# Performance work log

Hardware: AMD Instinct MI355X
Metric: run time of the kernel (lower is better)

## Reference

```python
import jax, jax.numpy as jnp
import numpy as np

N_NODES = 50000
N_EDGES = 800000
D = 128        # in_channels == out_channels
EDGE_DIM = 32
EPS = 0.0      # GINEConv default eps


def setup_inputs() -> dict:
    key = jax.random.key(0)
    ks = jax.random.split(key, 12)
    s = lambda d: 1.0 / np.sqrt(d)
    inp = {
        "x": jax.random.normal(ks[0], (N_NODES, D), jnp.float32),
        "edge_index": jax.random.randint(ks[1], (2, N_EDGES), 0, N_NODES, jnp.int64),
        "edge_attr": jax.random.normal(ks[2], (N_EDGES, EDGE_DIM), jnp.float32),
        "importance": jax.random.uniform(ks[3], (N_NODES, 1), jnp.float32),
        # GINEConv edge lin: Linear(edge_dim, in_channels)
        "We": jax.random.uniform(ks[4], (EDGE_DIM, D), jnp.float32, -s(EDGE_DIM), s(EDGE_DIM)),
        "be": jax.random.uniform(ks[5], (D,), jnp.float32, -s(EDGE_DIM), s(EDGE_DIM)),
        # GINEConv nn: Linear(in_channels, out_channels)
        "Wc": jax.random.uniform(ks[6], (D, D), jnp.float32, -s(D), s(D)),
        "bc": jax.random.uniform(ks[7], (D,), jnp.float32, -s(D), s(D)),
        # importance_gate: Linear(out_channels + 1, out_channels)
        "Wg": jax.random.uniform(ks[8], (D + 1, D), jnp.float32, -s(D + 1), s(D + 1)),
        "bg": jax.random.uniform(ks[9], (D,), jnp.float32, -s(D + 1), s(D + 1)),
        # importance_propagation: Linear(out_channels, 1)
        "Wp": jax.random.uniform(ks[10], (D, 1), jnp.float32, -s(D), s(D)),
        "bp": jax.random.uniform(ks[11], (1,), jnp.float32, -s(D), s(D)),
    }
    return inp


def reference(x, edge_index, edge_attr, importance, We, be, Wc, bc, Wg, bg, Wp, bp):
    src, dst = edge_index[0], edge_index[1]
    # GINEConv: messages = relu(x_j + lin(edge_attr)), aggregated by sum at dst
    e = edge_attr @ We + be                      # [E, D]
    msg = jax.nn.relu(x[src] + e)                # [E, D] gather + fused add/relu
    agg = jax.ops.segment_sum(msg, dst, num_segments=N_NODES)  # [N, D] scatter-add
    conv_out = ((1.0 + EPS) * x + agg) @ Wc + bc  # [N, D]
    # importance gating + residual
    gate_in = jnp.concatenate([conv_out, importance], axis=-1)  # [N, D+1]
    gate = jax.nn.sigmoid(gate_in @ Wg + bg)
    out = gate * conv_out + (1.0 - gate) * x
    propagated_importance = out @ Wp + bp        # [N, 1]
    return (out, propagated_importance)
```

## Files before the change

kernel.cpp:

```cpp
#include <hip/hip_runtime.h>

#define NN 50000
#define NE 800000
#define DD 128
#define ED 32
#define NB 196
#define NC32 (NE / 32)

typedef short  bf16x8 __attribute__((ext_vector_type(8)));
typedef float  f32x4  __attribute__((ext_vector_type(4)));
typedef float  f32x16 __attribute__((ext_vector_type(16)));

__device__ __forceinline__ float4 ld4(const float* p) {
    return *reinterpret_cast<const float4*>(p);
}
__device__ __forceinline__ short f2bf(float f) {
    unsigned u = __float_as_uint(f);
    u += 0x7fffu + ((u >> 16) & 1u);
    return (short)(u >> 16);
}
__device__ __forceinline__ float bf2f(short h) {
    return __uint_as_float(((unsigned)(unsigned short)h) << 16);
}
__device__ __forceinline__ int sniff64(const int* ei) {
    return ((ei[1] | ei[3] | ei[5] | ei[7]) == 0) ? 1 : 0;
}

__global__ __launch_bounds__(256)
void k_xcast(const float* __restrict__ x, unsigned int* __restrict__ xb) {
    const int t = blockIdx.x * 256 + threadIdx.x;
    if (t >= NN * 32) return;
    const int n = t >> 5, c = t & 31;
    const float* xr = x + (size_t)n * DD + c;
    const unsigned b0 = (unsigned short)f2bf(xr[0]);
    const unsigned b1 = (unsigned short)f2bf(xr[32]);
    const unsigned b2 = (unsigned short)f2bf(xr[64]);
    const unsigned b3 = (unsigned short)f2bf(xr[96]);
    xb[(size_t)n * 64 + c * 2]     = b0 | (b1 << 16);
    xb[(size_t)n * 64 + c * 2 + 1] = b2 | (b3 << 16);
}

__global__ __launch_bounds__(256)
void k_hist(const int* __restrict__ ei, int* __restrict__ counts) {
    const int is64 = sniff64(ei);
    const int2* ei2 = (const int2*)ei;
    for (int e = blockIdx.x * blockDim.x + threadIdx.x; e < NE;
         e += gridDim.x * blockDim.x) {
        const int dst = is64 ? ei2[NE + e].x : ei[NE + e];
        atomicAdd(&counts[dst], 1);
    }
}

__global__ __launch_bounds__(256)
void k_bsum(const int* __restrict__ counts, int* __restrict__ bsum) {
    const int i = blockIdx.x * 256 + threadIdx.x;
    int c = (i < NN) ? counts[i] : 0;
#pragma unroll
    for (int off = 32; off; off >>= 1) c += __shfl_xor(c, off, 64);
    __shared__ int ws4[4];
    if ((threadIdx.x & 63) == 0) ws4[threadIdx.x >> 6] = c;
    __syncthreads();
    if (threadIdx.x == 0) bsum[blockIdx.x] = ws4[0] + ws4[1] + ws4[2] + ws4[3];
}

__global__ __launch_bounds__(256)
void k_scanb(const int* __restrict__ bsum, int* __restrict__ bexcl) {
    const int tid = threadIdx.x, lane = tid & 63, w = tid >> 6;
    const int v = (tid < NB) ? bsum[tid] : 0;
    int s = v;
#pragma unroll
    for (int off = 1; off < 64; off <<= 1) {
        const int t = __shfl_up(s, off, 64);
        if (lane >= off) s += t;
    }
    __shared__ int wsum[4], wexcl[4];
    if (lane == 63) wsum[w] = s;
    __syncthreads();
    if (tid == 0) {
        int r = 0;
#pragma unroll
        for (int k = 0; k < 4; ++k) { wexcl[k] = r; r += wsum[k]; }
    }
    __syncthreads();
    if (tid < NB) bexcl[tid] = wexcl[w] + s - v;
}

__global__ __launch_bounds__(256)
void k_rowptr(const int* __restrict__ counts, const int* __restrict__ bexcl,
              int* __restrict__ cursor) {
    const int tid = threadIdx.x, lane = tid & 63, w = tid >> 6;
    const int i = blockIdx.x * 256 + tid;
    const int c = (i < NN) ? counts[i] : 0;
    int s = c;
#pragma unroll
    for (int off = 1; off < 64; off <<= 1) {
        const int t = __shfl_up(s, off, 64);
        if (lane >= off) s += t;
    }
    __shared__ int wsum[4], wexcl[4];
    if (lane == 63) wsum[w] = s;
    __syncthreads();
    if (tid == 0) {
        int r = 0;
#pragma unroll
        for (int k = 0; k < 4; ++k) { wexcl[k] = r; r += wsum[k]; }
    }
    __syncthreads();
    if (i < NN) cursor[i] = bexcl[blockIdx.x] + wexcl[w] + s - c;
}

__global__ __launch_bounds__(256)
void k_scatter2(const int* __restrict__ ei, int* __restrict__ cursor,
                const float* __restrict__ ea, int* __restrict__ sdat4,
                unsigned int* __restrict__ ebs)
{
    const int tid = threadIdx.x;
    const int e0  = blockIdx.x * 128;
    __shared__ int spos[128];
    if (tid < 128) {
        const int is64 = sniff64(ei);
        const int2* ei2 = (const int2*)ei;
        const int e   = e0 + tid;
        const int src = is64 ? ei2[e].x : ei[e];
        const int dst = is64 ? ei2[NE + e].x : ei[NE + e];
        const int pos = atomicAdd(&cursor[dst], 1);
        sdat4[pos] = src | (dst << 16);
        spos[tid] = pos;
    }
    __syncthreads();
#pragma unroll
    for (int it = 0; it < 8; ++it) {
        const int task = it * 256 + tid;
        const int el   = task >> 4;
        const int part = task & 15;
        const float2 v = *reinterpret_cast<const float2*>(
                             ea + (size_t)(e0 + el) * ED + part * 2);
        const unsigned lo = (unsigned short)f2bf(v.x);
        const unsigned hi = (unsigned short)f2bf(v.y);
        ebs[(size_t)spos[el] * 16 + part] = lo | (hi << 16);
    }
}

__global__ __launch_bounds__(256, 4)
void k_aggE(const unsigned int* __restrict__ xb, const unsigned int* __restrict__ ebs,
            const float* __restrict__ We, const float* __restrict__ be,
            const int* __restrict__ sdat4, float* __restrict__ agg)
{
    const int lane = threadIdx.x & 63;
    const int col  = lane & 31;
    const int h    = lane >> 5;
    const int wid  = (blockIdx.x << 2) | (threadIdx.x >> 6);

    bf16x8 Bf[4][2];
    float  beb[4];
#pragma unroll
    for (int bb = 0; bb < 4; ++bb) {
#pragma unroll
        for (int s = 0; s < 2; ++s)
#pragma unroll
            for (int i = 0; i < 8; ++i)
                Bf[bb][s][i] = f2bf(We[(s * 16 + h * 8 + i) * DD + bb * 32 + col]);
        beb[bb] = be[bb * 32 + col];
    }

    const int sd   = sdat4[wid * 32 + col];
    const int dstv = ((unsigned)sd) >> 16;

    const unsigned int* ebr = ebs + ((size_t)wid * 32 + col) * 16;
    const bf16x8 Af0 = *reinterpret_cast<const bf16x8*>(ebr + h * 4);
    const bf16x8 Af1 = *reinterpret_cast<const bf16x8*>(ebr + 8 + h * 4);

    f32x16 C[4];
#pragma unroll
    for (int reg = 0; reg < 16; ++reg) {
        const int E   = (reg & 3) + 8 * (reg >> 2) + 4 * h;
        const int src = __shfl(sd, E, 64) & 0xFFFF;
        const uint2 w = *reinterpret_cast<const uint2*>(
                            xb + (size_t)src * 64 + col * 2);
        C[0][reg] = __uint_as_float(w.x << 16);
        C[1][reg] = __uint_as_float(w.x & 0xFFFF0000u);
        C[2][reg] = __uint_as_float(w.y << 16);
        C[3][reg] = __uint_as_float(w.y & 0xFFFF0000u);
    }

#pragma unroll
    for (int bb = 0; bb < 4; ++bb) {
        C[bb] = __builtin_amdgcn_mfma_f32_32x32x16_bf16(Af0, Bf[bb][0], C[bb], 0, 0, 0);
        C[bb] = __builtin_amdgcn_mfma_f32_32x32x16_bf16(Af1, Bf[bb][1], C[bb], 0, 0, 0);
    }

#pragma unroll
    for (int bb = 0; bb < 4; ++bb)
#pragma unroll
        for (int reg = 0; reg < 16; ++reg)
            C[bb][reg] = fmaxf(C[bb][reg] + beb[bb], 0.0f);

    const int  prv  = __shfl(dstv, (lane == 0) ? 0 : lane - 1, 64);
    const bool flag = (lane < 32) && ((col == 0) || (dstv != prv));
    unsigned rem = (unsigned)(__ballot(flag) & 0xFFFFFFFFull);

    while (rem) {
        const int ms = __ffs((int)rem) - 1;
        rem &= rem - 1;
        const int hi = rem ? (__ffs((int)rem) - 1) : 32;
        const int d  = __shfl(dstv, ms, 64);

        float v0 = 0.f, v1 = 0.f, v2 = 0.f, v3 = 0.f;
#pragma unroll
        for (int reg = 0; reg < 16; ++reg) {
            const int E = (reg & 3) + 8 * (reg >> 2) + 4 * h;
            const float mk = (E >= ms && E < hi) ? 1.0f : 0.0f;
            v0 = fmaf(mk, C[0][reg], v0);
            v1 = fmaf(mk, C[1][reg], v1);
            v2 = fmaf(mk, C[2][reg], v2);
            v3 = fmaf(mk, C[3][reg], v3);
        }
        v0 += __shfl_xor(v0, 32, 64);
        v1 += __shfl_xor(v1, 32, 64);
        v2 += __shfl_xor(v2, 32, 64);
        v3 += __shfl_xor(v3, 32, 64);

        float* ar = agg + (size_t)d * DD + h * 64 + col;
        unsafeAtomicAdd(ar,      h ? v2 : v0);
        unsafeAtomicAdd(ar + 32, h ? v3 : v1);
    }
}

__global__ __launch_bounds__(256)
void k_cg(const float* __restrict__ x, const float* agg,
          const float* __restrict__ Wc, const float* __restrict__ bc,
          const float* __restrict__ imp, const float* __restrict__ Wg,
          const float* __restrict__ bg, const float* __restrict__ Wp,
          const float* __restrict__ bp, float* outp, float* __restrict__ prop)
{
    __shared__ short sBh[2048 * 8];
    __shared__ short sBl[2048 * 8];
    for (int idx = threadIdx.x; idx < 2048; idx += 256) {
        const int kk = idx >> 9;
        const int b  = (idx >> 6) & 7;
        const int l  = idx & 63;
        const int row0 = kk * 32 + ((l >> 4) << 3);
        const int col  = b * 16 + (l & 15);
        bf16x8 h8, l8;
#pragma unroll
        for (int j = 0; j < 8; ++j) {
            const float v = Wc[(row0 + j) * DD + col];
            const short h = f2bf(v);
            h8[j] = h;
            l8[j] = f2bf(v - bf2f(h));
        }
        *reinterpret_cast<bf16x8*>(&sBh[idx * 8]) = h8;
        *reinterpret_cast<bf16x8*>(&sBl[idx * 8]) = l8;
    }
    __syncthreads();

    const int lane = threadIdx.x & 63;
    const int ncol = lane & 15;
    const int krow = (lane >> 4) << 3;
    const int grp  = lane >> 4;
    const int wib  = threadIdx.x >> 6;
    const int wid  = (blockIdx.x << 2) | wib;
    const bool live = (wid < NN / 16);
    const int m0 = live ? wid * 16 : 0;

    f32x4 C[8];
#pragma unroll
    for (int b = 0; b < 8; ++b) {
        const float bcv = bc[b * 16 + ncol];
        f32x4 c = { bcv, bcv, bcv, bcv };
        C[b] = c;
    }
    {
        const float* xrow = x   + (size_t)(m0 + ncol) * DD + krow;
        const float* grow = agg + (size_t)(m0 + ncol) * DD + krow;
#pragma unroll
        for (int kk = 0; kk < 4; ++kk) {
            const float4 x0 = ld4(xrow + kk * 32), x1 = ld4(xrow + kk * 32 + 4);
            const float4 g0 = ld4(grow + kk * 32), g1 = ld4(grow + kk * 32 + 4);
            const float av[8] = { x0.x + g0.x, x0.y + g0.y, x0.z + g0.z, x0.w + g0.w,
                                  x1.x + g1.x, x1.y + g1.y, x1.z + g1.z, x1.w + g1.w };
            bf16x8 Ah, Al;
#pragma unroll
            for (int j = 0; j < 8; ++j) {
                const short h = f2bf(av[j]);
                Ah[j] = h;
                Al[j] = f2bf(av[j] - bf2f(h));
            }
#pragma unroll
            for (int b = 0; b < 8; ++b) {
                const bf16x8 Bh = *reinterpret_cast<const bf16x8*>(&sBh[((kk * 8 + b) * 64 + lane) * 8]);
                const bf16x8 Bl = *reinterpret_cast<const bf16x8*>(&sBl[((kk * 8 + b) * 64 + lane) * 8]);
                C[b] = __builtin_amdgcn_mfma_f32_16x16x32_bf16(Ah, Bh, C[b], 0, 0, 0);
                C[b] = __builtin_amdgcn_mfma_f32_16x16x32_bf16(Al, Bh, C[b], 0, 0, 0);
                C[b] = __builtin_amdgcn_mfma_f32_16x16x32_bf16(Ah, Bl, C[b], 0, 0, 0);
            }
        }
    }
    __syncthreads();

    for (int idx = threadIdx.x; idx < 2048; idx += 256) {
        const int kk = idx >> 9;
        const int b  = (idx >> 6) & 7;
        const int l  = idx & 63;
        const int row0 = kk * 32 + ((l >> 4) << 3);
        const int col  = b * 16 + (l & 15);
        bf16x8 h8;
#pragma unroll
        for (int j = 0; j < 8; ++j)
            h8[j] = f2bf(Wg[(row0 + j) * DD + col]);
        *reinterpret_cast<bf16x8*>(&sBh[idx * 8]) = h8;
    }
    float* scr = reinterpret_cast<float*>(sBl) + wib * 2048;
#pragma unroll
    for (int r = 0; r < 4; ++r)
#pragma unroll
        for (int b = 0; b < 8; ++b)
            scr[(grp * 4 + r) * DD + b * 16 + ncol] = C[b][r];
    __syncthreads();

    f32x4 Z[8];
#pragma unroll
    for (int b = 0; b < 8; ++b) {
        const float bgv = bg[b * 16 + ncol];
        f32x4 z = { bgv, bgv, bgv, bgv };
        Z[b] = z;
    }
#pragma unroll
    for (int kk = 0; kk < 4; ++kk) {
        const float4 a0 = ld4(scr + ncol * DD + kk * 32 + krow);
        const float4 a1 = ld4(scr + ncol * DD + kk * 32 + krow + 4);
        const float av[8] = { a0.x, a0.y, a0.z, a0.w, a1.x, a1.y, a1.z, a1.w };
        bf16x8 Ah;
#pragma unroll
        for (int j = 0; j < 8; ++j) Ah[j] = f2bf(av[j]);
#pragma unroll
        for (int b = 0; b < 8; ++b) {
            const bf16x8 Bh = *reinterpret_cast<const bf16x8*>(&sBh[((kk * 8 + b) * 64 + lane) * 8]);
            Z[b] = __builtin_amdgcn_mfma_f32_16x16x32_bf16(Ah, Bh, Z[b], 0, 0, 0);
        }
    }

    if (!live) return;

    float wgi[8], wp8[8];
#pragma unroll
    for (int b = 0; b < 8; ++b) {
        wgi[b] = Wg[DD * DD + b * 16 + ncol];
        wp8[b] = Wp[b * 16 + ncol];
    }
    const float bps = bp[0];

    float s[4] = { 0.f, 0.f, 0.f, 0.f };
#pragma unroll
    for (int r = 0; r < 4; ++r) {
        const int m = m0 + grp * 4 + r;
        const float im = imp[m];
        const float* xr = x + (size_t)m * DD + ncol;
        float* orow = outp + (size_t)m * DD + ncol;
#pragma unroll
        for (int b = 0; b < 8; ++b) {
            const float a = Z[b][r] + im * wgi[b];
            const float g = 1.0f / (1.0f + expf(-a));
            const float xv = xr[b * 16];
            const float o = fmaf(g, C[b][r] - xv, xv);
            orow[b * 16] = o;
            s[r] += o * wp8[b];
        }
    }
#pragma unroll
    for (int off = 1; off < 16; off <<= 1) {
        s[0] += __shfl_xor(s[0], off, 64);
        s[1] += __shfl_xor(s[1], off, 64);
        s[2] += __shfl_xor(s[2], off, 64);
        s[3] += __shfl_xor(s[3], off, 64);
    }
    if (ncol < 4) {
        const float v = (ncol == 0) ? s[0] : (ncol == 1) ? s[1] : (ncol == 2) ? s[2] : s[3];
        prop[m0 + grp * 4 + ncol] = v + bps;
    }
}

extern "C" void kernel_launch(void* const* d_in, const int* in_sizes, int n_in,
                              void* d_out, int out_size, void* d_ws, size_t ws_size,
                              hipStream_t stream) {
    const float* x   = (const float*)d_in[0];
    const int*   ei  = (const int*)d_in[1];
    const float* ea  = (const float*)d_in[2];
    const float* imp = (const float*)d_in[3];
    const float* We  = (const float*)d_in[4];
    const float* be  = (const float*)d_in[5];
    const float* Wc  = (const float*)d_in[6];
    const float* bc  = (const float*)d_in[7];
    const float* Wg  = (const float*)d_in[8];
    const float* bg  = (const float*)d_in[9];
    const float* Wp  = (const float*)d_in[10];
    const float* bp  = (const float*)d_in[11];

    float* out  = (float*)d_out;
    float* prop = out + (size_t)NN * DD;
    float* agg  = out;

    int*          counts = (int*)d_ws;
    int*          cursor = (int*)((char*)d_ws + 204800);
    int*          bsum   = (int*)((char*)d_ws + 409600);
    int*          bexcl  = (int*)((char*)d_ws + 413696);
    int*          sdat4  = (int*)((char*)d_ws + 1048576);
    unsigned int* xb     = (unsigned int*)((char*)d_ws + 4456448);
    unsigned int* ebs    = (unsigned int*)((char*)d_ws + 17301504);

    hipMemsetAsync(counts, 0, NN * sizeof(int), stream);
    hipMemsetAsync(agg, 0, (size_t)NN * DD * sizeof(float), stream);
    hipLaunchKernelGGL(k_xcast,    dim3(6250), dim3(256), 0, stream, x, xb);
    hipLaunchKernelGGL(k_hist,     dim3(2048), dim3(256), 0, stream, ei, counts);
    hipLaunchKernelGGL(k_bsum,     dim3(NB),   dim3(256), 0, stream, counts, bsum);
    hipLaunchKernelGGL(k_scanb,    dim3(1),    dim3(256), 0, stream, bsum, bexcl);
    hipLaunchKernelGGL(k_rowptr,   dim3(NB),   dim3(256), 0, stream, counts, bexcl, cursor);
    hipLaunchKernelGGL(k_scatter2, dim3(6250), dim3(256), 0, stream, ei, cursor, ea, sdat4, ebs);
    hipLaunchKernelGGL(k_aggE,     dim3(6250), dim3(256), 0, stream,
                       xb, ebs, We, be, sdat4, agg);
    hipLaunchKernelGGL(k_cg,       dim3(782),  dim3(256), 0, stream,
                       x, agg, Wc, bc, imp, Wg, bg, Wp, bp, out, prop);
}
```

Before: 216.3 us.

## Fuse setup kernels, precompute bf16 We fragments, and pipeline two edge chunks per wave

Merges the x-to-bf16 cast, the destination histogram and a one-time bf16 conversion of We into a single setup kernel. The aggregation kernel then loads prebuilt We fragments instead of converting them in every wave. Each wave now handles two 32-edge chunks, issuing the second chunk's x gathers before the first chunk's atomic epilogue so memory latency overlaps the atomics. The cost is more registers (launch bounds relaxed to 2) and therefore lower occupancy.

```diff
diff --git a/kernel.cpp b/kernel.cpp
--- a/kernel.cpp
+++ b/kernel.cpp
@@ -5,7 +5,6 @@
 #define DD 128
 #define ED 32
 #define NB 196
-#define NC32 (NE / 32)
 
 typedef short  bf16x8 __attribute__((ext_vector_type(8)));
 typedef float  f32x4  __attribute__((ext_vector_type(4)));
@@ -27,27 +26,39 @@
 }
 
 __global__ __launch_bounds__(256)
-void k_xcast(const float* __restrict__ x, unsigned int* __restrict__ xb) {
-    const int t = blockIdx.x * 256 + threadIdx.x;
-    if (t >= NN * 32) return;
-    const int n = t >> 5, c = t & 31;
-    const float* xr = x + (size_t)n * DD + c;
-    const unsigned b0 = (unsigned short)f2bf(xr[0]);
-    const unsigned b1 = (unsigned short)f2bf(xr[32]);
-    const unsigned b2 = (unsigned short)f2bf(xr[64]);
-    const unsigned b3 = (unsigned short)f2bf(xr[96]);
-    xb[(size_t)n * 64 + c * 2]     = b0 | (b1 << 16);
-    xb[(size_t)n * 64 + c * 2 + 1] = b2 | (b3 << 16);
-}
-
-__global__ __launch_bounds__(256)
-void k_hist(const int* __restrict__ ei, int* __restrict__ counts) {
-    const int is64 = sniff64(ei);
-    const int2* ei2 = (const int2*)ei;
-    for (int e = blockIdx.x * blockDim.x + threadIdx.x; e < NE;
-         e += gridDim.x * blockDim.x) {
-        const int dst = is64 ? ei2[NE + e].x : ei[NE + e];
-        atomicAdd(&counts[dst], 1);
+void k_setup(const float* __restrict__ x, const int* __restrict__ ei,
+             const float* __restrict__ We, unsigned int* __restrict__ xb,
+             int* __restrict__ counts, unsigned short* __restrict__ Bft)
+{
+    const int tid = threadIdx.x;
+    if (blockIdx.x < 6250) {
+        const int t = blockIdx.x * 256 + tid;
+        if (t >= NN * 32) return;
+        const int n = t >> 5, c = t & 31;
+        const float* xr = x + (size_t)n * DD + c;
+        const unsigned b0 = (unsigned short)f2bf(xr[0]);
+        const unsigned b1 = (unsigned short)f2bf(xr[32]);
+        const unsigned b2 = (unsigned short)f2bf(xr[64]);
+        const unsigned b3 = (unsigned short)f2bf(xr[96]);
+        xb[(size_t)n * 64 + c * 2]     = b0 | (b1 << 16);
+        xb[(size_t)n * 64 + c * 2 + 1] = b2 | (b3 << 16);
+    } else if (blockIdx.x < 8298) {
+        const int is64 = sniff64(ei);
+        const int2* ei2 = (const int2*)ei;
+        for (int e = (blockIdx.x - 6250) * 256 + tid; e < NE; e += 2048 * 256) {
+            const int dst = is64 ? ei2[NE + e].x : ei[NE + e];
+            atomicAdd(&counts[dst], 1);
+        }
+    } else if (tid < 64) {
+        const int col = tid & 31, h = tid >> 5;
+#pragma unroll
+        for (int bb = 0; bb < 4; ++bb)
+#pragma unroll
+            for (int s = 0; s < 2; ++s)
+#pragma unroll
+                for (int i = 0; i < 8; ++i)
+                    Bft[tid * 64 + (bb * 2 + s) * 8 + i] =
+                        (unsigned short)f2bf(We[(s * 16 + h * 8 + i) * DD + bb * 32 + col]);
     }
 }
 
@@ -141,54 +152,10 @@
     }
 }
 
-__global__ __launch_bounds__(256, 4)
-void k_aggE(const unsigned int* __restrict__ xb, const unsigned int* __restrict__ ebs,
-            const float* __restrict__ We, const float* __restrict__ be,
-            const int* __restrict__ sdat4, float* __restrict__ agg)
+__device__ __forceinline__ void agg_epilogue(f32x16 (&C)[4], const float beb[4],
+                                             int dstv, int lane, int col, int h,
+                                             float* __restrict__ agg)
 {
-    const int lane = threadIdx.x & 63;
-    const int col  = lane & 31;
-    const int h    = lane >> 5;
-    const int wid  = (blockIdx.x << 2) | (threadIdx.x >> 6);
-
-    bf16x8 Bf[4][2];
-    float  beb[4];
-#pragma unroll
-    for (int bb = 0; bb < 4; ++bb) {
-#pragma unroll
-        for (int s = 0; s < 2; ++s)
-#pragma unroll
-            for (int i = 0; i < 8; ++i)
-                Bf[bb][s][i] = f2bf(We[(s * 16 + h * 8 + i) * DD + bb * 32 + col]);
-        beb[bb] = be[bb * 32 + col];
-    }
-
-    const int sd   = sdat4[wid * 32 + col];
-    const int dstv = ((unsigned)sd) >> 16;
-
-    const unsigned int* ebr = ebs + ((size_t)wid * 32 + col) * 16;
-    const bf16x8 Af0 = *reinterpret_cast<const bf16x8*>(ebr + h * 4);
-    const bf16x8 Af1 = *reinterpret_cast<const bf16x8*>(ebr + 8 + h * 4);
-
-    f32x16 C[4];
-#pragma unroll
-    for (int reg = 0; reg < 16; ++reg) {
-        const int E   = (reg & 3) + 8 * (reg >> 2) + 4 * h;
-        const int src = __shfl(sd, E, 64) & 0xFFFF;
-        const uint2 w = *reinterpret_cast<const uint2*>(
-                            xb + (size_t)src * 64 + col * 2);
-        C[0][reg] = __uint_as_float(w.x << 16);
-        C[1][reg] = __uint_as_float(w.x & 0xFFFF0000u);
-        C[2][reg] = __uint_as_float(w.y << 16);
-        C[3][reg] = __uint_as_float(w.y & 0xFFFF0000u);
-    }
-
-#pragma unroll
-    for (int bb = 0; bb < 4; ++bb) {
-        C[bb] = __builtin_amdgcn_mfma_f32_32x32x16_bf16(Af0, Bf[bb][0], C[bb], 0, 0, 0);
-        C[bb] = __builtin_amdgcn_mfma_f32_32x32x16_bf16(Af1, Bf[bb][1], C[bb], 0, 0, 0);
-    }
-
 #pragma unroll
     for (int bb = 0; bb < 4; ++bb)
 #pragma unroll
@@ -224,6 +191,86 @@
         unsafeAtomicAdd(ar,      h ? v2 : v0);
         unsafeAtomicAdd(ar + 32, h ? v3 : v1);
     }
+}
+
+__global__ __launch_bounds__(256, 2)
+void k_aggE(const unsigned int* __restrict__ xb, const unsigned int* __restrict__ ebs,
+            const unsigned short* __restrict__ Bft, const float* __restrict__ be,
+            const int* __restrict__ sdat4, float* __restrict__ agg)
+{
+    const int lane = threadIdx.x & 63;
+    const int col  = lane & 31;
+    const int h    = lane >> 5;
+    const int wid  = (blockIdx.x << 2) | (threadIdx.x >> 6);
+    const int c0   = wid * 2, c1 = wid * 2 + 1;
+
+    bf16x8 Bf[4][2];
+    {
+        const bf16x8* bp_ = reinterpret_cast<const bf16x8*>(Bft + lane * 64);
+#pragma unroll
+        for (int bb = 0; bb < 4; ++bb) {
+            Bf[bb][0] = bp_[bb * 2];
+            Bf[bb][1] = bp_[bb * 2 + 1];
+        }
+    }
+    float beb[4];
+#pragma unroll
+    for (int bb = 0; bb < 4; ++bb) beb[bb] = be[bb * 32 + col];
+
+    const int sd0 = sdat4[c0 * 32 + col];
+    const int sd1 = sdat4[c1 * 32 + col];
+    const unsigned int* ebr0 = ebs + ((size_t)c0 * 32 + col) * 16;
+    const unsigned int* ebr1 = ebs + ((size_t)c1 * 32 + col) * 16;
+    const bf16x8 A00 = *reinterpret_cast<const bf16x8*>(ebr0 + h * 4);
+    const bf16x8 A01 = *reinterpret_cast<const bf16x8*>(ebr0 + 8 + h * 4);
+    const bf16x8 A10 = *reinterpret_cast<const bf16x8*>(ebr1 + h * 4);
+    const bf16x8 A11 = *reinterpret_cast<const bf16x8*>(ebr1 + 8 + h * 4);
+
+    uint2 w0[16];
+#pragma unroll
+    for (int reg = 0; reg < 16; ++reg) {
+        const int E   = (reg & 3) + 8 * (reg >> 2) + 4 * h;
+        const int src = __shfl(sd0, E, 64) & 0xFFFF;
+        w0[reg] = *reinterpret_cast<const uint2*>(xb + (size_t)src * 64 + col * 2);
+    }
+
+    f32x16 C[4];
+#pragma unroll
+    for (int reg = 0; reg < 16; ++reg) {
+        C[0][reg] = __uint_as_float(w0[reg].x << 16);
+        C[1][reg] = __uint_as_float(w0[reg].x & 0xFFFF0000u);
+        C[2][reg] = __uint_as_float(w0[reg].y << 16);
+        C[3][reg] = __uint_as_float(w0[reg].y & 0xFFFF0000u);
+    }
+#pragma unroll
+    for (int bb = 0; bb < 4; ++bb) {
+        C[bb] = __builtin_amdgcn_mfma_f32_32x32x16_bf16(A00, Bf[bb][0], C[bb], 0, 0, 0);
+        C[bb] = __builtin_amdgcn_mfma_f32_32x32x16_bf16(A01, Bf[bb][1], C[bb], 0, 0, 0);
+    }
+
+    uint2 w1[16];
+#pragma unroll
+    for (int reg = 0; reg < 16; ++reg) {
+        const int E   = (reg & 3) + 8 * (reg >> 2) + 4 * h;
+        const int src = __shfl(sd1, E, 64) & 0xFFFF;
+        w1[reg] = *reinterpret_cast<const uint2*>(xb + (size_t)src * 64 + col * 2);
+    }
+
+    agg_epilogue(C, beb, ((unsigned)sd0) >> 16, lane, col, h, agg);
+
+#pragma unroll
+    for (int reg = 0; reg < 16; ++reg) {
+        C[0][reg] = __uint_as_float(w1[reg].x << 16);
+        C[1][reg] = __uint_as_float(w1[reg].x & 0xFFFF0000u);
+        C[2][reg] = __uint_as_float(w1[reg].y << 16);
+        C[3][reg] = __uint_as_float(w1[reg].y & 0xFFFF0000u);
+    }
+#pragma unroll
+    for (int bb = 0; bb < 4; ++bb) {
+        C[bb] = __builtin_amdgcn_mfma_f32_32x32x16_bf16(A10, Bf[bb][0], C[bb], 0, 0, 0);
+        C[bb] = __builtin_amdgcn_mfma_f32_32x32x16_bf16(A11, Bf[bb][1], C[bb], 0, 0, 0);
+    }
+    agg_epilogue(C, beb, ((unsigned)sd1) >> 16, lane, col, h, agg);
 }
 
 __global__ __launch_bounds__(256)
@@ -400,24 +447,25 @@
     float* prop = out + (size_t)NN * DD;
     float* agg  = out;
 
-    int*          counts = (int*)d_ws;
-    int*          cursor = (int*)((char*)d_ws + 204800);
-    int*          bsum   = (int*)((char*)d_ws + 409600);
-    int*          bexcl  = (int*)((char*)d_ws + 413696);
-    int*          sdat4  = (int*)((char*)d_ws + 1048576);
-    unsigned int* xb     = (unsigned int*)((char*)d_ws + 4456448);
-    unsigned int* ebs    = (unsigned int*)((char*)d_ws + 17301504);
+    int*            counts = (int*)d_ws;
+    int*            cursor = (int*)((char*)d_ws + 204800);
+    int*            bsum   = (int*)((char*)d_ws + 409600);
+    int*            bexcl  = (int*)((char*)d_ws + 413696);
+    unsigned short* Bft    = (unsigned short*)((char*)d_ws + 417792);
+    int*            sdat4  = (int*)((char*)d_ws + 1048576);
+    unsigned int*   xb     = (unsigned int*)((char*)d_ws + 4456448);
+    unsigned int*   ebs    = (unsigned int*)((char*)d_ws + 17301504);
 
     hipMemsetAsync(counts, 0, NN * sizeof(int), stream);
     hipMemsetAsync(agg, 0, (size_t)NN * DD * sizeof(float), stream);
-    hipLaunchKernelGGL(k_xcast,    dim3(6250), dim3(256), 0, stream, x, xb);
-    hipLaunchKernelGGL(k_hist,     dim3(2048), dim3(256), 0, stream, ei, counts);
+    hipLaunchKernelGGL(k_setup,    dim3(8299), dim3(256), 0, stream,
+                       x, ei, We, xb, counts, Bft);
     hipLaunchKernelGGL(k_bsum,     dim3(NB),   dim3(256), 0, stream, counts, bsum);
     hipLaunchKernelGGL(k_scanb,    dim3(1),    dim3(256), 0, stream, bsum, bexcl);
     hipLaunchKernelGGL(k_rowptr,   dim3(NB),   dim3(256), 0, stream, counts, bexcl, cursor);
     hipLaunchKernelGGL(k_scatter2, dim3(6250), dim3(256), 0, stream, ei, cursor, ea, sdat4, ebs);
-    hipLaunchKernelGGL(k_aggE,     dim3(6250), dim3(256), 0, stream,
-                       xb, ebs, We, be, sdat4, agg);
+    hipLaunchKernelGGL(k_aggE,     dim3(3125), dim3(256), 0, stream,
+                       xb, ebs, Bft, be, sdat4, agg);
     hipLaunchKernelGGL(k_cg,       dim3(782),  dim3(256), 0, stream,
                        x, agg, Wc, bc, imp, Wg, bg, Wp, bp, out, prop);
 }
```

Result: faster. 207.1 us (-4.2%).
